# Optimization experiments

Hardware: AMD Instinct MI355X
Metric: run time of the kernel (lower is better)

## Reference

```python
import jax, jax.numpy as jnp
import numpy as np

B, L, C = 2, 2048, 1024
H = 16
D = C // H  # 64
MAX_SCALE_MUL = float(np.log(100.0))
EPS = 1e-12


def setup_inputs() -> dict:
    key = jax.random.key(0)
    ks = jax.random.split(key, 6)
    x = jax.random.normal(ks[0], (B, L, C), dtype=jnp.float32)
    attn_bias = jax.random.normal(ks[1], (1, 1, L, L), dtype=jnp.float32) * 0.02
    W_qkv = jax.random.normal(ks[2], (3 * C, C), dtype=jnp.float32) * (1.0 / np.sqrt(C))
    q_bias = jnp.zeros((C,), dtype=jnp.float32)
    v_bias = jnp.zeros((C,), dtype=jnp.float32)
    scale_mul = jnp.full((1, H, 1, 1), np.log(4.0), dtype=jnp.float32)
    W_proj = jax.random.normal(ks[3], (C, C), dtype=jnp.float32) * (1.0 / np.sqrt(C))
    b_proj = jnp.zeros((C,), dtype=jnp.float32)
    return {"x": x, "attn_bias": attn_bias, "W_qkv": W_qkv, "q_bias": q_bias,
            "v_bias": v_bias, "scale_mul": scale_mul, "W_proj": W_proj, "b_proj": b_proj}


def _l2norm(t):
    # F.normalize(dim=-1): x / max(||x||_2, eps)
    n = jnp.sqrt(jnp.sum(t * t, axis=-1, keepdims=True))
    return t / jnp.maximum(n, EPS)


def reference(x, attn_bias, W_qkv, q_bias, v_bias, scale_mul, W_proj, b_proj):
    bias = jnp.concatenate([q_bias, jnp.zeros_like(q_bias), v_bias])  # (3C,)
    qkv = x @ W_qkv.T + bias                     # (B, L, 3C)
    qkv = qkv.reshape(B, L, 3, H, D)
    q, k, v = jnp.moveaxis(qkv, 2, 0)            # each (B, L, H, D)
    q = jnp.transpose(q, (0, 2, 1, 3))           # (B, H, L, D)
    k = jnp.transpose(k, (0, 2, 1, 3))
    v = jnp.transpose(v, (0, 2, 1, 3))
    # attn_l2_norm path: scale = 1, learned per-head scale clamped at log(100)
    sm = jnp.exp(jnp.minimum(scale_mul, MAX_SCALE_MUL))  # (1, H, 1, 1)
    q = _l2norm(q) * sm
    k = _l2norm(k)
    scores = jnp.einsum('bhqd,bhkd->bhqk', q, k) + attn_bias  # scale=1
    attn = jax.nn.softmax(scores, axis=-1)
    out = jnp.einsum('bhqk,bhkd->bhqd', attn, v)  # (B, H, L, D)
    out = jnp.transpose(out, (0, 2, 1, 3)).reshape(B, L, C)
    return out @ W_proj.T + b_proj
```

## Files before the change

kernel.cpp:

```cpp
#include <hip/hip_runtime.h>


typedef __bf16 bf16x8 __attribute__((ext_vector_type(8)));
typedef __bf16 bf16x4 __attribute__((ext_vector_type(4)));
typedef float  f32x4  __attribute__((ext_vector_type(4)));

#define BB 2
#define LL 2048
#define CC 1024
#define HH 16
#define DD 64
#define LOG2E 1.44269504088896f

__device__ __forceinline__ f32x4 mfma_16x16x32(bf16x8 a, bf16x8 b, f32x4 c) {
    return __builtin_amdgcn_mfma_f32_16x16x32_bf16(a, b, c, 0, 0, 0);
}

__device__ __forceinline__ void gload_lds16(const __bf16* g, __bf16* lds) {
    __builtin_amdgcn_global_load_lds(
        (const __attribute__((address_space(1))) unsigned int*)g,
        (__attribute__((address_space(3))) unsigned int*)lds,
        16, 0, 0);
}

__device__ __forceinline__ unsigned pk_bf16(float a, float b) {
    unsigned short ua = __builtin_bit_cast(unsigned short, (__bf16)a);
    unsigned short ub = __builtin_bit_cast(unsigned short, (__bf16)b);
    return (unsigned)ua | ((unsigned)ub << 16);
}

__global__ __launch_bounds__(256) void cvt_bf16_kernel(const float* __restrict__ in,
                                                       __bf16* __restrict__ out, int n4) {
    int i = blockIdx.x * 256 + threadIdx.x;
    if (i >= n4) return;
    float4 v = reinterpret_cast<const float4*>(in)[i];
    bf16x4 o;
    o[0] = (__bf16)v.x; o[1] = (__bf16)v.y; o[2] = (__bf16)v.z; o[3] = (__bf16)v.w;
    reinterpret_cast<bf16x4*>(out)[i] = o;
}

__global__ __launch_bounds__(256) void bias_prep_kernel(const float* __restrict__ bias,
                                                        __bf16* __restrict__ bias_bf) {
    __shared__ float wmax[4];
    const int l = blockIdx.x, tid = threadIdx.x;
    const int w = tid >> 6;
    float4 a = reinterpret_cast<const float4*>(bias + (size_t)l * 2048)[tid];
    float4 b = reinterpret_cast<const float4*>(bias + (size_t)l * 2048 + 1024)[tid];
    float m = fmaxf(fmaxf(fmaxf(a.x, a.y), fmaxf(a.z, a.w)),
                    fmaxf(fmaxf(b.x, b.y), fmaxf(b.z, b.w)));
#pragma unroll
    for (int off = 1; off < 64; off <<= 1) m = fmaxf(m, __shfl_xor(m, off, 64));
    if ((tid & 63) == 0) wmax[w] = m;
    __syncthreads();
    float M = fmaxf(fmaxf(wmax[0], wmax[1]), fmaxf(wmax[2], wmax[3]));
    bf16x4 o0, o1;
    o0[0] = (__bf16)((a.x - M) * LOG2E); o0[1] = (__bf16)((a.y - M) * LOG2E);
    o0[2] = (__bf16)((a.z - M) * LOG2E); o0[3] = (__bf16)((a.w - M) * LOG2E);
    o1[0] = (__bf16)((b.x - M) * LOG2E); o1[1] = (__bf16)((b.y - M) * LOG2E);
    o1[2] = (__bf16)((b.z - M) * LOG2E); o1[3] = (__bf16)((b.w - M) * LOG2E);
    reinterpret_cast<bf16x4*>(bias_bf + (size_t)l * 2048)[tid] = o0;
    reinterpret_cast<bf16x4*>(bias_bf + (size_t)l * 2048 + 1024)[tid] = o1;
}

template <int OUT_MODE>
__global__ __launch_bounds__(256) void gemm_bt_kernel(
    const __bf16* __restrict__ A, const __bf16* __restrict__ Bm,
    float* __restrict__ Cf, __bf16* __restrict__ Cb,
    const float* __restrict__ bias, int M, int N, int K) {
    __shared__ __bf16 As[128 * 64];
    __shared__ __bf16 Bs[128 * 64];
    const int tid = threadIdx.x;
    const int nwg = gridDim.x * gridDim.y;
    const int flat = blockIdx.y * gridDim.x + blockIdx.x;
    const int wg = (flat & 7) * (nwg >> 3) + (flat >> 3);
    const int m0 = (wg % gridDim.x) * 128, n0 = (wg / gridDim.x) * 128;
    const int w  = tid >> 6, l = tid & 63;
    const int wr = (w >> 1) * 64, wc = (w & 1) * 64;
    const int lr = l & 15, lg = l >> 4;
    const int rmask = (lr & 7) << 4;
    f32x4 acc[4][4] = {};
    const int lrow = l >> 3;
    const int celem = (((l & 7) ^ lrow) << 3);

    for (int kt = 0; kt < K; kt += 64) {
        __syncthreads();
#pragma unroll
        for (int i = 0; i < 4; ++i) {
            const int row = w * 32 + i * 8;
            gload_lds16(A + (size_t)(m0 + row + lrow) * K + kt + celem, &As[row * 64]);
            gload_lds16(Bm + (size_t)(n0 + row + lrow) * K + kt + celem, &Bs[row * 64]);
        }
        asm volatile("s_waitcnt vmcnt(0)" ::: "memory");
        __syncthreads();
#pragma unroll
        for (int kk = 0; kk < 2; ++kk) {
            bf16x8 af[4], bfr[4];
#pragma unroll
            for (int m = 0; m < 4; ++m)
                af[m] = *reinterpret_cast<const bf16x8*>(
                    (char*)As + (wr + m * 16 + lr) * 128 + ((kk * 64 + lg * 16) ^ rmask));
#pragma unroll
            for (int n = 0; n < 4; ++n)
                bfr[n] = *reinterpret_cast<const bf16x8*>(
                    (char*)Bs + (wc + n * 16 + lr) * 128 + ((kk * 64 + lg * 16) ^ rmask));
#pragma unroll
            for (int m = 0; m < 4; ++m)
#pragma unroll
                for (int n = 0; n < 4; ++n)
                    acc[m][n] = mfma_16x16x32(af[m], bfr[n], acc[m][n]);
        }
    }
#pragma unroll
    for (int m = 0; m < 4; ++m) {
#pragma unroll
        for (int n = 0; n < 4; ++n) {
            const int row = m0 + wr + m * 16 + lg * 4;
            const int col = n0 + wc + n * 16 + lr;
#pragma unroll
            for (int r = 0; r < 4; ++r) {
                float v = acc[m][n][r];
                if (OUT_MODE == 0) {
                    Cb[(size_t)(row + r) * N + col] = (__bf16)v;
                } else {
                    Cf[(size_t)(row + r) * N + col] = v + bias[col];
                }
            }
        }
    }
}

__global__ __launch_bounds__(256) void qkv_norm_kernel(
    const __bf16* __restrict__ qkv, const float* __restrict__ q_bias,
    const float* __restrict__ v_bias, const float* __restrict__ scale_mul,
    __bf16* __restrict__ Q, __bf16* __restrict__ K, __bf16* __restrict__ V) {
    const int bl = blockIdx.x;
    const int tid = threadIdx.x;
    const int w = tid >> 6, d = tid & 63;
    const int b = bl >> 11, l = bl & 2047;
    for (int g = w; g < 48; g += 4) {
        const int s = g >> 4, h = g & 15;
        float v = (float)qkv[(size_t)bl * 3072 + g * 64 + d];
        if (s == 0) v += q_bias[h * 64 + d];
        if (s == 2) v += v_bias[h * 64 + d];
        if (s < 2) {
            float ss = v * v;
#pragma unroll
            for (int off = 1; off < 64; off <<= 1) ss += __shfl_xor(ss, off, 64);
            float nrm = sqrtf(ss);
            v = v / fmaxf(nrm, 1e-12f);
            if (s == 0) v *= __expf(fminf(scale_mul[h], 4.60517019f)) * LOG2E;
        }
        __bf16* dst = (s == 0) ? Q : ((s == 1) ? K : V);
        dst[((size_t)(b * 16 + h) * 2048 + l) * 64 + d] = (__bf16)v;
    }
}

__global__ __launch_bounds__(256) void v_transpose_kernel(const __bf16* __restrict__ Vin,
                                                          __bf16* __restrict__ Vt) {
    __shared__ __bf16 T[64][72];
    const int lb = blockIdx.x, bh = blockIdx.y;
    const int tid = threadIdx.x;
    const size_t base = (size_t)bh * LL * DD;
    const int row = tid >> 2, c = (tid & 3) * 16;
    {
        const __bf16* src = Vin + base + (size_t)(lb * 64 + row) * 64 + c;
        *reinterpret_cast<bf16x8*>(&T[row][c])     = *reinterpret_cast<const bf16x8*>(src);
        *reinterpret_cast<bf16x8*>(&T[row][c + 8]) = *reinterpret_cast<const bf16x8*>(src + 8);
    }
    __syncthreads();
    bf16x8 o0, o1;
#pragma unroll
    for (int j = 0; j < 8; ++j) {
        o0[j] = T[c + j][row];
        o1[j] = T[c + 8 + j][row];
    }
    __bf16* dst = Vt + base + (size_t)row * 2048 + lb * 64 + c;
    *reinterpret_cast<bf16x8*>(dst)     = o0;
    *reinterpret_cast<bf16x8*>(dst + 8) = o1;
}

__global__ __launch_bounds__(256, 4) void attn_kernel(
    const __bf16* __restrict__ Q, const __bf16* __restrict__ K,
    const __bf16* __restrict__ Vt, const __bf16* __restrict__ biasL,
    const float* __restrict__ scale_mul, __bf16* __restrict__ Octx) {
    __shared__ __bf16 KVs[2][2][64 * 64];
    const int bh = blockIdx.x, qb = blockIdx.y;
    const int tid = threadIdx.x;
    const int w = tid >> 6, l = tid & 63;
    const int lr = l & 15, lg = l >> 4;
    const int rmask = (lr & 7) << 4;
    const int b = bh >> 4, h = bh & 15;
    const size_t base = (size_t)bh * LL * DD;
    const float smh = __expf(fminf(scale_mul[h], 4.60517019f));
    const float cexp = -smh * LOG2E;

    const int gq = qb * 64 + w * 16 + lr;
    bf16x8 qf[2];
    qf[0] = *reinterpret_cast<const bf16x8*>(Q + base + (size_t)gq * 64 + lg * 8);
    qf[1] = *reinterpret_cast<const bf16x8*>(Q + base + (size_t)gq * 64 + 32 + lg * 8);
    const __bf16* brow = biasL + (size_t)gq * 2048 + lg * 4;

    const int srow = tid >> 2;
    const int scb  = (tid & 3) * 32;
    const int smask = (srow & 7) << 4;
    const __bf16* kgbase = K  + base + (size_t)srow * 64   + (tid & 3) * 16;
    const __bf16* vgbase = Vt + base + (size_t)srow * 2048 + (tid & 3) * 16;

    bf16x8 k0, k1, v0, v1;
    auto stage_regs = [&](int kb) {
        const __bf16* kg = kgbase + (size_t)kb * 64 * 64;
        k0 = *reinterpret_cast<const bf16x8*>(kg);
        k1 = *reinterpret_cast<const bf16x8*>(kg + 8);
        const __bf16* vg = vgbase + kb * 64;
        v0 = *reinterpret_cast<const bf16x8*>(vg);
        v1 = *reinterpret_cast<const bf16x8*>(vg + 8);
    };
    auto write_lds = [&](int buf) {
        char* kp = (char*)KVs[buf][0] + srow * 128;
        char* vp = (char*)KVs[buf][1] + srow * 128;
        *reinterpret_cast<bf16x8*>(kp + (scb ^ smask))        = k0;
        *reinterpret_cast<bf16x8*>(kp + ((scb + 16) ^ smask)) = k1;
        *reinterpret_cast<bf16x8*>(vp + (scb ^ smask))        = v0;
        *reinterpret_cast<bf16x8*>(vp + ((scb + 16) ^ smask)) = v1;
    };

    stage_regs(0);
    write_lds(0);

    f32x4 Oa[4] = {};
    float lsum = 0.f;
    int cur = 0;

    bf16x4 bcur[4];
#pragma unroll
    for (int t = 0; t < 4; ++t)
        bcur[t] = *reinterpret_cast<const bf16x4*>(brow + t * 16);

    for (int kb = 0; kb < 32; ++kb) {
        __syncthreads();
        if (kb < 31) stage_regs(kb + 1);

        bf16x4 bnext[4];
        if (kb < 31) {
#pragma unroll
            for (int t = 0; t < 4; ++t)
                bnext[t] = *reinterpret_cast<const bf16x4*>(brow + (kb + 1) * 64 + t * 16);
        }

        const char* Kc = (const char*)KVs[cur][0];
        const char* Vc = (const char*)KVs[cur][1];

        f32x4 sa[4];
#pragma unroll
        for (int t = 0; t < 4; ++t)
#pragma unroll
            for (int r = 0; r < 4; ++r)
                sa[t][r] = (float)bcur[t][r] + cexp;

#pragma unroll
        for (int t = 0; t < 4; ++t) {
            const char* kr = Kc + (t * 16 + lr) * 128;
            bf16x8 kf0 = *reinterpret_cast<const bf16x8*>(kr + ((lg * 16) ^ rmask));
            bf16x8 kf1 = *reinterpret_cast<const bf16x8*>(kr + ((64 + lg * 16) ^ rmask));
            sa[t] = mfma_16x16x32(kf0, qf[0], sa[t]);
            sa[t] = mfma_16x16x32(kf1, qf[1], sa[t]);
        }

        float p[4][4];
#pragma unroll
        for (int t = 0; t < 4; ++t)
#pragma unroll
            for (int r = 0; r < 4; ++r) {
                p[t][r] = exp2f(sa[t][r]);
                lsum += p[t][r];
            }
        union Upa { unsigned u[4]; bf16x8 v; } pa0, pa1;
        pa0.u[0] = pk_bf16(p[0][0], p[0][1]); pa0.u[1] = pk_bf16(p[0][2], p[0][3]);
        pa0.u[2] = pk_bf16(p[1][0], p[1][1]); pa0.u[3] = pk_bf16(p[1][2], p[1][3]);
        pa1.u[0] = pk_bf16(p[2][0], p[2][1]); pa1.u[1] = pk_bf16(p[2][2], p[2][3]);
        pa1.u[2] = pk_bf16(p[3][0], p[3][1]); pa1.u[3] = pk_bf16(p[3][2], p[3][3]);

#pragma unroll
        for (int t = 0; t < 4; ++t) {
            const char* vr = Vc + (t * 16 + lr) * 128;
            union Uv { uint2 d[2]; bf16x8 v; } vf0, vf1;
            vf0.d[0] = *reinterpret_cast<const uint2*>(vr + ((lg * 8) ^ rmask));
            vf0.d[1] = *reinterpret_cast<const uint2*>(vr + ((32 + lg * 8) ^ rmask));
            vf1.d[0] = *reinterpret_cast<const uint2*>(vr + ((64 + lg * 8) ^ rmask));
            vf1.d[1] = *reinterpret_cast<const uint2*>(vr + ((96 + lg * 8) ^ rmask));
            Oa[t] = mfma_16x16x32(pa0.v, vf0.v, Oa[t]);
            Oa[t] = mfma_16x16x32(pa1.v, vf1.v, Oa[t]);
        }

        if (kb < 31) {
            write_lds(cur ^ 1);
#pragma unroll
            for (int t = 0; t < 4; ++t) bcur[t] = bnext[t];
        }
        cur ^= 1;
    }

    lsum += __shfl_xor(lsum, 16, 64);
    lsum += __shfl_xor(lsum, 32, 64);
    float inv[4];
#pragma unroll
    for (int r = 0; r < 4; ++r) inv[r] = 1.0f / __shfl(lsum, lg * 4 + r, 64);

#pragma unroll
    for (int t = 0; t < 4; ++t)
#pragma unroll
        for (int r = 0; r < 4; ++r) {
            const int row = qb * 64 + w * 16 + lg * 4 + r;
            float o = Oa[t][r] * inv[r];
            Octx[((size_t)(b * 2048 + row)) * 1024 + h * 64 + t * 16 + lr] = (__bf16)o;
        }
}

extern "C" void kernel_launch(void* const* d_in, const int* in_sizes, int n_in,
                              void* d_out, int out_size, void* d_ws, size_t ws_size,
                              hipStream_t stream) {
    const float* x         = (const float*)d_in[0];
    const float* attn_bias = (const float*)d_in[1];
    const float* W_qkv     = (const float*)d_in[2];
    const float* q_bias    = (const float*)d_in[3];
    const float* v_bias    = (const float*)d_in[4];
    const float* scale_mul = (const float*)d_in[5];
    const float* W_proj    = (const float*)d_in[6];
    const float* b_proj    = (const float*)d_in[7];
    float* out = (float*)d_out;

    char* ws = (char*)d_ws;
    size_t off = 0;
    auto alloc = [&](size_t bytes) {
        void* p = ws + off;
        off = (off + bytes + 255) & ~(size_t)255;
        return p;
    };
    __bf16* xb     = (__bf16*)alloc((size_t)4096 * 1024 * 2);
    __bf16* wqkvb  = (__bf16*)alloc((size_t)3072 * 1024 * 2);
    __bf16* wprojb = (__bf16*)alloc((size_t)1024 * 1024 * 2);
    __bf16* qkvb   = (__bf16*)alloc((size_t)4096 * 3072 * 2);
    __bf16* Qw     = (__bf16*)alloc((size_t)BB * HH * LL * DD * 2);
    __bf16* Kw     = (__bf16*)alloc((size_t)BB * HH * LL * DD * 2);
    __bf16* Vw     = (__bf16*)alloc((size_t)BB * HH * LL * DD * 2);
    __bf16* Oc     = (__bf16*)alloc((size_t)4096 * 1024 * 2);
    __bf16* bias_bf = qkvb;
    __bf16* Vt      = qkvb + (size_t)2048 * 2048;

    cvt_bf16_kernel<<<4096, 256, 0, stream>>>(x, xb, 4096 * 1024 / 4);
    cvt_bf16_kernel<<<3072, 256, 0, stream>>>(W_qkv, wqkvb, 3072 * 1024 / 4);
    cvt_bf16_kernel<<<1024, 256, 0, stream>>>(W_proj, wprojb, 1024 * 1024 / 4);

    gemm_bt_kernel<0><<<dim3(32, 24), 256, 0, stream>>>(
        xb, wqkvb, nullptr, qkvb, nullptr, 4096, 3072, 1024);

    qkv_norm_kernel<<<4096, 256, 0, stream>>>(qkvb, q_bias, v_bias, scale_mul, Qw, Kw, Vw);

    bias_prep_kernel<<<2048, 256, 0, stream>>>(attn_bias, bias_bf);
    v_transpose_kernel<<<dim3(32, 32), 256, 0, stream>>>(Vw, Vt);

    attn_kernel<<<dim3(32, 32), 256, 0, stream>>>(Qw, Kw, Vt, bias_bf, scale_mul, Oc);

    gemm_bt_kernel<1><<<dim3(32, 8), 256, 0, stream>>>(
        Oc, wprojb, out, nullptr, b_proj, 4096, 1024, 1024);
}
```

Measured before the change: 197.7 us.

## Fuse QKV bias, L2 norm and head scatter into QKV GEMM epilogue

Folds the q/v bias add, per-head L2 normalisation, the learned scale and the scatter into (B,H,L,D) layout into the QKV GEMM epilogue. Each wave's 64 output columns are exactly one head, so the row norm is reduced with lane shuffles. This removes the separate qkv_norm kernel and the round trip of the 24MB bf16 qkv intermediate. It also adds s_setprio around the MFMA blocks in the attention kernel, and gives bias_bf and Vt their own workspace buffers instead of aliasing qkvb. The epilogue stores are scattered 2-byte writes, which may coalesce poorly.

```diff
diff --git a/kernel.cpp b/kernel.cpp
--- a/kernel.cpp
+++ b/kernel.cpp
@@ -62,11 +62,112 @@
     reinterpret_cast<bf16x4*>(bias_bf + (size_t)l * 2048 + 1024)[tid] = o1;
 }
 
-template <int OUT_MODE>
-__global__ __launch_bounds__(256) void gemm_bt_kernel(
+__global__ __launch_bounds__(256) void gemm_qkv_fused_kernel(
     const __bf16* __restrict__ A, const __bf16* __restrict__ Bm,
-    float* __restrict__ Cf, __bf16* __restrict__ Cb,
-    const float* __restrict__ bias, int M, int N, int K) {
+    const float* __restrict__ q_bias, const float* __restrict__ v_bias,
+    const float* __restrict__ scale_mul,
+    __bf16* __restrict__ Qw, __bf16* __restrict__ Kw, __bf16* __restrict__ Vw) {
+    __shared__ __bf16 As[128 * 64];
+    __shared__ __bf16 Bs[128 * 64];
+    const int tid = threadIdx.x;
+    const int K = 1024;
+    const int nwg = gridDim.x * gridDim.y;
+    const int flat = blockIdx.y * gridDim.x + blockIdx.x;
+    const int wg = (flat & 7) * (nwg >> 3) + (flat >> 3);
+    const int m0 = (wg % gridDim.x) * 128, n0 = (wg / gridDim.x) * 128;
+    const int w  = tid >> 6, l = tid & 63;
+    const int wr = (w >> 1) * 64, wc = (w & 1) * 64;
+    const int lr = l & 15, lg = l >> 4;
+    const int rmask = (lr & 7) << 4;
+    f32x4 acc[4][4] = {};
+    const int lrow = l >> 3;
+    const int celem = (((l & 7) ^ lrow) << 3);
+
+    for (int kt = 0; kt < K; kt += 64) {
+        __syncthreads();
+#pragma unroll
+        for (int i = 0; i < 4; ++i) {
+            const int row = w * 32 + i * 8;
+            gload_lds16(A + (size_t)(m0 + row + lrow) * K + kt + celem, &As[row * 64]);
+            gload_lds16(Bm + (size_t)(n0 + row + lrow) * K + kt + celem, &Bs[row * 64]);
+        }
+        asm volatile("s_waitcnt vmcnt(0)" ::: "memory");
+        __syncthreads();
+#pragma unroll
+        for (int kk = 0; kk < 2; ++kk) {
+            bf16x8 af[4], bfr[4];
+#pragma unroll
+            for (int m = 0; m < 4; ++m)
+                af[m] = *reinterpret_cast<const bf16x8*>(
+                    (char*)As + (wr + m * 16 + lr) * 128 + ((kk * 64 + lg * 16) ^ rmask));
+#pragma unroll
+            for (int n = 0; n < 4; ++n)
+                bfr[n] = *reinterpret_cast<const bf16x8*>(
+                    (char*)Bs + (wc + n * 16 + lr) * 128 + ((kk * 64 + lg * 16) ^ rmask));
+#pragma unroll
+            for (int m = 0; m < 4; ++m)
+#pragma unroll
+                for (int n = 0; n < 4; ++n)
+                    acc[m][n] = mfma_16x16x32(af[m], bfr[n], acc[m][n]);
+        }
+    }
+
+    const int gcbase = n0 + wc;
+    const int type = gcbase >> 10;
+    const int h = (gcbase & 1023) >> 6;
+    float qscale = 1.0f;
+    if (type == 0) qscale = __expf(fminf(scale_mul[h], 4.60517019f)) * LOG2E;
+    __bf16* dst = (type == 0) ? Qw : (type == 1) ? Kw : Vw;
+
+#pragma unroll
+    for (int m = 0; m < 4; ++m) {
+        if (type != 1) {
+            const float* bptr = (type == 0) ? q_bias : v_bias;
+#pragma unroll
+            for (int n = 0; n < 4; ++n) {
+                float bv = bptr[(gcbase & 1023) + n * 16 + lr];
+#pragma unroll
+                for (int r = 0; r < 4; ++r) acc[m][n][r] += bv;
+            }
+        }
+        float rs[4];
+        if (type < 2) {
+#pragma unroll
+            for (int r = 0; r < 4; ++r) {
+                float ss = 0.f;
+#pragma unroll
+                for (int n = 0; n < 4; ++n) ss += acc[m][n][r] * acc[m][n][r];
+                rs[r] = ss;
+            }
+#pragma unroll
+            for (int off = 1; off < 16; off <<= 1)
+#pragma unroll
+                for (int r = 0; r < 4; ++r) rs[r] += __shfl_xor(rs[r], off, 64);
+#pragma unroll
+            for (int r = 0; r < 4; ++r)
+                rs[r] = ((type == 0) ? qscale : 1.0f) / fmaxf(sqrtf(rs[r]), 1e-12f);
+        } else {
+#pragma unroll
+            for (int r = 0; r < 4; ++r) rs[r] = 1.0f;
+        }
+        const int rowg = m0 + wr + m * 16 + lg * 4;
+#pragma unroll
+        for (int n = 0; n < 4; ++n) {
+            const int d = n * 16 + lr;
+#pragma unroll
+            for (int r = 0; r < 4; ++r) {
+                const int row = rowg + r;
+                const int bb = row >> 11, ll = row & 2047;
+                dst[((size_t)((bb << 4) + h) * 2048 + ll) * 64 + d] =
+                    (__bf16)(acc[m][n][r] * rs[r]);
+            }
+        }
+    }
+}
+
+__global__ __launch_bounds__(256) void gemm_proj_kernel(
+    const __bf16* __restrict__ A, const __bf16* __restrict__ Bm,
+    float* __restrict__ Cf, const float* __restrict__ bias, int M, int N, int K) {
     __shared__ __bf16 As[128 * 64];
     __shared__ __bf16 Bs[128 * 64];
     const int tid = threadIdx.x;
@@ -111,48 +212,15 @@
         }
     }
 #pragma unroll
-    for (int m = 0; m < 4; ++m) {
+    for (int m = 0; m < 4; ++m)
 #pragma unroll
         for (int n = 0; n < 4; ++n) {
             const int row = m0 + wr + m * 16 + lg * 4;
             const int col = n0 + wc + n * 16 + lr;
 #pragma unroll
-            for (int r = 0; r < 4; ++r) {
-                float v = acc[m][n][r];
-                if (OUT_MODE == 0) {
-                    Cb[(size_t)(row + r) * N + col] = (__bf16)v;
-                } else {
-                    Cf[(size_t)(row + r) * N + col] = v + bias[col];
-                }
-            }
-        }
-    }
-}
-
-__global__ __launch_bounds__(256) void qkv_norm_kernel(
-    const __bf16* __restrict__ qkv, const float* __restrict__ q_bias,
-    const float* __restrict__ v_bias, const float* __restrict__ scale_mul,
-    __bf16* __restrict__ Q, __bf16* __restrict__ K, __bf16* __restrict__ V) {
-    const int bl = blockIdx.x;
-    const int tid = threadIdx.x;
-    const int w = tid >> 6, d = tid & 63;
-    const int b = bl >> 11, l = bl & 2047;
-    for (int g = w; g < 48; g += 4) {
-        const int s = g >> 4, h = g & 15;
-        float v = (float)qkv[(size_t)bl * 3072 + g * 64 + d];
-        if (s == 0) v += q_bias[h * 64 + d];
-        if (s == 2) v += v_bias[h * 64 + d];
-        if (s < 2) {
-            float ss = v * v;
-#pragma unroll
-            for (int off = 1; off < 64; off <<= 1) ss += __shfl_xor(ss, off, 64);
-            float nrm = sqrtf(ss);
-            v = v / fmaxf(nrm, 1e-12f);
-            if (s == 0) v *= __expf(fminf(scale_mul[h], 4.60517019f)) * LOG2E;
-        }
-        __bf16* dst = (s == 0) ? Q : ((s == 1) ? K : V);
-        dst[((size_t)(b * 16 + h) * 2048 + l) * 64 + d] = (__bf16)v;
-    }
+            for (int r = 0; r < 4; ++r)
+                Cf[(size_t)(row + r) * N + col] = acc[m][n][r] + bias[col];
+        }
 }
 
 __global__ __launch_bounds__(256) void v_transpose_kernel(const __bf16* __restrict__ Vin,
@@ -257,6 +325,7 @@
             for (int r = 0; r < 4; ++r)
                 sa[t][r] = (float)bcur[t][r] + cexp;
 
+        __builtin_amdgcn_s_setprio(1);
 #pragma unroll
         for (int t = 0; t < 4; ++t) {
             const char* kr = Kc + (t * 16 + lr) * 128;
@@ -265,6 +334,7 @@
             sa[t] = mfma_16x16x32(kf0, qf[0], sa[t]);
             sa[t] = mfma_16x16x32(kf1, qf[1], sa[t]);
         }
+        __builtin_amdgcn_s_setprio(0);
 
         float p[4][4];
 #pragma unroll
@@ -280,6 +350,7 @@
         pa1.u[0] = pk_bf16(p[2][0], p[2][1]); pa1.u[1] = pk_bf16(p[2][2], p[2][3]);
         pa1.u[2] = pk_bf16(p[3][0], p[3][1]); pa1.u[3] = pk_bf16(p[3][2], p[3][3]);
 
+        __builtin_amdgcn_s_setprio(1);
 #pragma unroll
         for (int t = 0; t < 4; ++t) {
             const char* vr = Vc + (t * 16 + lr) * 128;
@@ -291,6 +362,7 @@
             Oa[t] = mfma_16x16x32(pa0.v, vf0.v, Oa[t]);
             Oa[t] = mfma_16x16x32(pa1.v, vf1.v, Oa[t]);
         }
+        __builtin_amdgcn_s_setprio(0);
 
         if (kb < 31) {
             write_lds(cur ^ 1);
@@ -336,31 +408,28 @@
         off = (off + bytes + 255) & ~(size_t)255;
         return p;
     };
-    __bf16* xb     = (__bf16*)alloc((size_t)4096 * 1024 * 2);
-    __bf16* wqkvb  = (__bf16*)alloc((size_t)3072 * 1024 * 2);
-    __bf16* wprojb = (__bf16*)alloc((size_t)1024 * 1024 * 2);
-    __bf16* qkvb   = (__bf16*)alloc((size_t)4096 * 3072 * 2);
-    __bf16* Qw     = (__bf16*)alloc((size_t)BB * HH * LL * DD * 2);
-    __bf16* Kw     = (__bf16*)alloc((size_t)BB * HH * LL * DD * 2);
-    __bf16* Vw     = (__bf16*)alloc((size_t)BB * HH * LL * DD * 2);
-    __bf16* Oc     = (__bf16*)alloc((size_t)4096 * 1024 * 2);
-    __bf16* bias_bf = qkvb;
-    __bf16* Vt      = qkvb + (size_t)2048 * 2048;
+    __bf16* xb      = (__bf16*)alloc((size_t)4096 * 1024 * 2);
+    __bf16* wqkvb   = (__bf16*)alloc((size_t)3072 * 1024 * 2);
+    __bf16* wprojb  = (__bf16*)alloc((size_t)1024 * 1024 * 2);
+    __bf16* Qw      = (__bf16*)alloc((size_t)BB * HH * LL * DD * 2);
+    __bf16* Kw      = (__bf16*)alloc((size_t)BB * HH * LL * DD * 2);
+    __bf16* Vw      = (__bf16*)alloc((size_t)BB * HH * LL * DD * 2);
+    __bf16* Oc      = (__bf16*)alloc((size_t)4096 * 1024 * 2);
+    __bf16* bias_bf = (__bf16*)alloc((size_t)2048 * 2048 * 2);
+    __bf16* Vt      = (__bf16*)alloc((size_t)BB * HH * LL * DD * 2);
 
     cvt_bf16_kernel<<<4096, 256, 0, stream>>>(x, xb, 4096 * 1024 / 4);
     cvt_bf16_kernel<<<3072, 256, 0, stream>>>(W_qkv, wqkvb, 3072 * 1024 / 4);
     cvt_bf16_kernel<<<1024, 256, 0, stream>>>(W_proj, wprojb, 1024 * 1024 / 4);
 
-    gemm_bt_kernel<0><<<dim3(32, 24), 256, 0, stream>>>(
-        xb, wqkvb, nullptr, qkvb, nullptr, 4096, 3072, 1024);
-
-    qkv_norm_kernel<<<4096, 256, 0, stream>>>(qkvb, q_bias, v_bias, scale_mul, Qw, Kw, Vw);
+    gemm_qkv_fused_kernel<<<dim3(32, 24), 256, 0, stream>>>(
+        xb, wqkvb, q_bias, v_bias, scale_mul, Qw, Kw, Vw);
 
     bias_prep_kernel<<<2048, 256, 0, stream>>>(attn_bias, bias_bf);
     v_transpose_kernel<<<dim3(32, 32), 256, 0, stream>>>(Vw, Vt);
 
     attn_kernel<<<dim3(32, 32), 256, 0, stream>>>(Qw, Kw, Vt, bias_bf, scale_mul, Oc);
 
-    gemm_bt_kernel<1><<<dim3(32, 8), 256, 0, stream>>>(
-        Oc, wprojb, out, nullptr, b_proj, 4096, 1024, 1024);
-}
+    gemm_proj_kernel<<<dim3(32, 8), 256, 0, stream>>>(
+        Oc, wprojb, out, b_proj, 4096, 1024, 1024);
+}
```

Result: faster. 187.1 us (-5.3%).
